# Performance work log

Measured on AMD Instinct MI355X. Metric: run time of the kernel, lower is better.

The kernel has to match this reference:

```python
import jax, jax.numpy as jnp
import numpy as np

N = 50000        # nodes
E = 800000       # edges
IN_C = 128       # in_channels
HID = 256        # hidden_channels
HEADS = 4
HD = HID // HEADS
LAYERS = 4
GRAPHS = 64
OUT_C = 32
MAX_POS = 10
EPS = 1e-5


def layer_norm(x, g, b):
    mu = jnp.mean(x, axis=-1, keepdims=True)
    var = jnp.mean((x - mu) ** 2, axis=-1, keepdims=True)
    return (x - mu) / jnp.sqrt(var + EPS) * g + b


def setup_inputs() -> dict:
    key = jax.random.key(0)
    ks = jax.random.split(key, 32)
    s = 0.02
    inp = {
        "x": jax.random.normal(ks[0], (N, IN_C), dtype=jnp.float32),
        "edge_index": jax.random.randint(ks[1], (2, E), 0, N, dtype=jnp.int32),
        "pos_idx": jax.random.randint(ks[2], (N,), 0, MAX_POS, dtype=jnp.int32),
        "batch": jnp.sort(jax.random.randint(ks[3], (N,), 0, GRAPHS, dtype=jnp.int32)),
        # encoder MLP: Linear(IN->HID), ReLU, LN(HID), Linear(HID->HID); weights stored [in,out]
        "enc_w1": jax.random.normal(ks[4], (IN_C, HID)) * s,
        "enc_b1": jnp.zeros((HID,), jnp.float32),
        "enc_g": jnp.ones((HID,), jnp.float32),
        "enc_beta": jnp.zeros((HID,), jnp.float32),
        "enc_w2": jax.random.normal(ks[5], (HID, HID)) * s,
        "enc_b2": jnp.zeros((HID,), jnp.float32),
        "pos_emb": jax.random.normal(ks[6], (MAX_POS, HID)) * s,
        # stacked attention-layer params [LAYERS, ...]
        "Wq": jax.random.normal(ks[7], (LAYERS, HID, HID)) * s,
        "bq": jnp.zeros((LAYERS, HID), jnp.float32),
        "Wk": jax.random.normal(ks[8], (LAYERS, HID, HID)) * s,
        "bk": jnp.zeros((LAYERS, HID), jnp.float32),
        "Wv": jax.random.normal(ks[9], (LAYERS, HID, HID)) * s,
        "bv": jnp.zeros((LAYERS, HID), jnp.float32),
        "mlp_w1": jax.random.normal(ks[10], (LAYERS, 2 * HID, HID)) * s,
        "mlp_b1": jnp.zeros((LAYERS, HID), jnp.float32),
        "mlp_g": jnp.ones((LAYERS, HID), jnp.float32),
        "mlp_beta": jnp.zeros((LAYERS, HID), jnp.float32),
        "mlp_w2": jax.random.normal(ks[11], (LAYERS, HID, HID)) * s,
        "mlp_b2": jnp.zeros((LAYERS, HID), jnp.float32),
        # classifier
        "cls_w1": jax.random.normal(ks[12], (HID, HID)) * s,
        "cls_b1": jnp.zeros((HID,), jnp.float32),
        "cls_g": jnp.ones((HID,), jnp.float32),
        "cls_beta": jnp.zeros((HID,), jnp.float32),
        "cls_w2": jax.random.normal(ks[13], (HID, OUT_C)) * s,
        "cls_b2": jnp.zeros((OUT_C,), jnp.float32),
    }
    return inp


def reference(x, edge_index, pos_idx, batch,
              enc_w1, enc_b1, enc_g, enc_beta, enc_w2, enc_b2, pos_emb,
              Wq, bq, Wk, bk, Wv, bv,
              mlp_w1, mlp_b1, mlp_g, mlp_beta, mlp_w2, mlp_b2,
              cls_w1, cls_b1, cls_g, cls_beta, cls_w2, cls_b2):
    row, col = edge_index[0], edge_index[1]
    n = x.shape[0]
    e = row.shape[0]

    # NodeEncoder
    h = layer_norm(jax.nn.relu(x @ enc_w1 + enc_b1), enc_g, enc_beta) @ enc_w2 + enc_b2
    h = h + pos_emb[pos_idx]

    scale = jnp.asarray(HD, h.dtype) ** 0.5
    for l in range(LAYERS):
        Q = (h @ Wq[l] + bq[l]).reshape(n, HEADS, HD)
        K = (h @ Wk[l] + bk[l]).reshape(n, HEADS, HD)
        V = (h @ Wv[l] + bv[l]).reshape(n, HEADS, HD)
        # per-edge attention scores [E, HEADS]
        scores = jnp.sum(Q[row] * K[col], axis=-1) / scale
        # segment softmax over destination node `row`
        m = jax.ops.segment_max(scores, row, num_segments=n)
        ex = jnp.exp(scores - m[row])
        denom = jax.ops.segment_sum(ex, row, num_segments=n)
        w = ex / denom[row]                         # [E, HEADS]
        msg = (w[..., None] * V[col]).reshape(e, HID)
        agg = jax.ops.segment_sum(msg, row, num_segments=n)  # [N, HID]
        cat = jnp.concatenate([h, agg], axis=-1)
        z = layer_norm(jax.nn.relu(cat @ mlp_w1[l] + mlp_b1[l]), mlp_g[l], mlp_beta[l]) @ mlp_w2[l] + mlp_b2[l]
        h = z + h

    # global mean pool over graphs
    sums = jax.ops.segment_sum(h, batch, num_segments=GRAPHS)
    cnt = jax.ops.segment_sum(jnp.ones((n, 1), h.dtype), batch, num_segments=GRAPHS)
    pooled = sums / jnp.maximum(cnt, 1.0)

    out = layer_norm(jax.nn.relu(pooled @ cls_w1 + cls_b1), cls_g, cls_beta) @ cls_w2 + cls_b2
    return out
```

## Files before the change

kernel.cpp:

```cpp
#include <hip/hip_runtime.h>
#include <cstdint>

#define HID 256
#define HEADS 4
#define GRAPHS 64
#define OUTC 32
#define EPSV 1e-5f
#define PSPLIT 32

typedef __bf16 b16x8 __attribute__((ext_vector_type(8)));
typedef float  f32x4 __attribute__((ext_vector_type(4)));

__device__ __forceinline__ f32x4 mfma16(b16x8 a, b16x8 b, f32x4 c) {
    return __builtin_amdgcn_mfma_f32_16x16x32_bf16(a, b, c, 0, 0, 0);
}

__device__ __forceinline__ unsigned int pack_bf16(float a, float b) {
    unsigned short ua = __builtin_bit_cast(unsigned short, (__bf16)a);
    unsigned short ub = __builtin_bit_cast(unsigned short, (__bf16)b);
    return (unsigned int)ua | ((unsigned int)ub << 16);
}

__device__ __forceinline__ void unpack2(unsigned int u, float& lo, float& hi) {
    lo = __builtin_bit_cast(float, u << 16);
    hi = __builtin_bit_cast(float, u & 0xffff0000u);
}

__device__ __forceinline__ void stage_gld(char* buf, const unsigned short* __restrict__ src,
                                          int base, int tid)
{
#pragma unroll
    for (int i = 0; i < 8; i++) {
        int idx = i * 256 + tid;
        int r = idx >> 5;
        int u = idx & 31;
        int us = u ^ (r & 7);
        const void* gp = (const void*)(src + (size_t)(base + r) * HID + us * 8);
        __builtin_amdgcn_global_load_lds(
            (const __attribute__((address_space(1))) void*)gp,
            (__attribute__((address_space(3))) void*)(buf + idx * 16),
            16, 0, 0);
    }
}

__global__ __launch_bounds__(256) void wtrans_kernel(const float* __restrict__ W,
    unsigned short* __restrict__ Wt, int K, int C)
{
    __shared__ float tile[32][33];
    const float* Wm = W + (size_t)blockIdx.z * K * C;
    unsigned short* Wtm = Wt + (size_t)blockIdx.z * K * C;
    int k0 = blockIdx.x * 32, c0 = blockIdx.y * 32;
    int tx = threadIdx.x & 31, ty = threadIdx.x >> 5;
#pragma unroll
    for (int i = 0; i < 32; i += 8)
        tile[ty + i][tx] = Wm[(size_t)(k0 + ty + i) * C + c0 + tx];
    __syncthreads();
#pragma unroll
    for (int i = 0; i < 32; i += 8) {
        float v = tile[tx][ty + i];
        Wtm[(size_t)(c0 + ty + i) * K + k0 + tx] =
            __builtin_bit_cast(unsigned short, (__bf16)v);
    }
}

__global__ __launch_bounds__(256) void enc1_mfma(
    const float* __restrict__ in0, const unsigned short* __restrict__ Wt,
    const float* __restrict__ bias, const float* __restrict__ g,
    const float* __restrict__ be, unsigned short* __restrict__ outb, int n)
{
    constexpr int KTILE = 128, ROWB = 256;
    __shared__ __align__(16) char alds[64 * 256];
    __shared__ float red[4][64][2];
    int tid = threadIdx.x, lane = tid & 63, wv = tid >> 6;
    int cg = lane & 15, rg = lane >> 4;
    int base = blockIdx.x * 64;
    int cbase = wv * 64;

    f32x4 acc[4][4];
#pragma unroll
    for (int m = 0; m < 4; m++)
#pragma unroll
        for (int f = 0; f < 4; f++) acc[m][f] = (f32x4){0.f, 0.f, 0.f, 0.f};

#pragma unroll
    for (int i = 0; i < 8; i++) {
        int idx = (i * 256 + tid) * 4;
        int row = idx >> 7, k = idx & 127;
        int node = base + row;
        float4 v = {0.f, 0.f, 0.f, 0.f};
        if (node < n) v = *(const float4*)(in0 + (size_t)node * KTILE + k);
        uint2 pp; pp.x = pack_bf16(v.x, v.y); pp.y = pack_bf16(v.z, v.w);
        int off = row * ROWB + k * 2;
        off ^= (row & 7) << 4;
        *(uint2*)(alds + off) = pp;
    }
    __syncthreads();

#pragma unroll 2
    for (int k0 = 0; k0 < KTILE; k0 += 32) {
        b16x8 a[4], b[4];
#pragma unroll
        for (int m = 0; m < 4; m++) {
            int R = m * 16 + cg;
            int off = R * ROWB + (k0 + rg * 8) * 2;
            off ^= (R & 7) << 4;
            a[m] = __builtin_bit_cast(b16x8, *(const uint4*)(alds + off));
        }
#pragma unroll
        for (int f = 0; f < 4; f++) {
            const unsigned short* p = Wt + (size_t)(cbase + f * 16 + cg) * KTILE + k0 + rg * 8;
            b[f] = __builtin_bit_cast(b16x8, *(const uint4*)p);
        }
#pragma unroll
        for (int m = 0; m < 4; m++)
#pragma unroll
            for (int f = 0; f < 4; f++)
                acc[m][f] = mfma16(a[m], b[f], acc[m][f]);
    }

    float bias_v[4], g_v[4], be_v[4];
#pragma unroll
    for (int f = 0; f < 4; f++) {
        int col = cbase + f * 16 + cg;
        bias_v[f] = bias[col]; g_v[f] = g[col]; be_v[f] = be[col];
    }
#pragma unroll
    for (int m = 0; m < 4; m++)
#pragma unroll
        for (int f = 0; f < 4; f++)
#pragma unroll
            for (int r = 0; r < 4; r++)
                acc[m][f][r] = fmaxf(acc[m][f][r] + bias_v[f], 0.f);
#pragma unroll
    for (int m = 0; m < 4; m++)
#pragma unroll
        for (int r = 0; r < 4; r++) {
            float s = acc[m][0][r] + acc[m][1][r] + acc[m][2][r] + acc[m][3][r];
            float q = acc[m][0][r] * acc[m][0][r] + acc[m][1][r] * acc[m][1][r]
                    + acc[m][2][r] * acc[m][2][r] + acc[m][3][r] * acc[m][3][r];
#pragma unroll
            for (int o = 1; o < 16; o <<= 1) {
                s += __shfl_xor(s, o, 64); q += __shfl_xor(q, o, 64);
            }
            if (cg == 0) { int R = m * 16 + rg * 4 + r; red[wv][R][0] = s; red[wv][R][1] = q; }
        }
    __syncthreads();
#pragma unroll
    for (int m = 0; m < 4; m++)
#pragma unroll
        for (int r = 0; r < 4; r++) {
            int R = m * 16 + rg * 4 + r;
            float S = red[0][R][0] + red[1][R][0] + red[2][R][0] + red[3][R][0];
            float Q = red[0][R][1] + red[1][R][1] + red[2][R][1] + red[3][R][1];
            float mu = S * (1.f / HID);
            float rs = rsqrtf(Q * (1.f / HID) - mu * mu + EPSV);
            int row = base + R;
            if (row >= n) continue;
            size_t ro = (size_t)row * HID;
#pragma unroll
            for (int f = 0; f < 4; f++) {
                float v = (acc[m][f][r] - mu) * rs * g_v[f] + be_v[f];
                outb[ro + cbase + f * 16 + cg] = __builtin_bit_cast(unsigned short, (__bf16)v);
            }
        }
}

template<int NPASS, bool RELU_LN, bool ADD_RES, bool POS, bool OUTF, bool OUTB>
__global__ __launch_bounds__(256) void gemm_bf16(
    const unsigned short* __restrict__ in0, const unsigned short* __restrict__ in1,
    const unsigned short* __restrict__ Wt, const float* __restrict__ bias,
    const float* __restrict__ g, const float* __restrict__ be,
    const float* __restrict__ addsrc, const float* __restrict__ pos_emb,
    const int* __restrict__ pidx, float* __restrict__ outf,
    unsigned short* __restrict__ outb, int n)
{
    constexpr int KTILE = 256;
    constexpr int KS = KTILE * NPASS;
    __shared__ __align__(16) char alds[64 * 512];
    __shared__ float red[4][64][2];

    int tid = threadIdx.x, lane = tid & 63, wv = tid >> 6;
    int cg = lane & 15, rg = lane >> 4;
    int base = blockIdx.x * 64;
    int cbase = wv * 64;

    f32x4 acc[4][4];
#pragma unroll
    for (int m = 0; m < 4; m++)
#pragma unroll
        for (int f = 0; f < 4; f++) acc[m][f] = (f32x4){0.f, 0.f, 0.f, 0.f};

    for (int pass = 0; pass < NPASS; pass++) {
        if (pass) __syncthreads();
        const unsigned short* src = pass ? in1 : in0;
        const unsigned short* Wp = Wt + pass * KTILE;

        stage_gld(alds, src, base, tid);

        b16x8 bcur[4], bnxt[4];
#pragma unroll
        for (int f = 0; f < 4; f++)
            bcur[f] = __builtin_bit_cast(b16x8, *(const uint4*)(
                Wp + (size_t)(cbase + f * 16 + cg) * KS + rg * 8));
        __syncthreads();

#pragma unroll
        for (int kk = 0; kk < 8; kk++) {
            if (kk < 7) {
#pragma unroll
                for (int f = 0; f < 4; f++)
                    bnxt[f] = __builtin_bit_cast(b16x8, *(const uint4*)(
                        Wp + (size_t)(cbase + f * 16 + cg) * KS + (kk + 1) * 32 + rg * 8));
            }
            b16x8 a[4];
#pragma unroll
            for (int m = 0; m < 4; m++) {
                int R = m * 16 + cg;
                int off = R * 512 + (kk * 32 + rg * 8) * 2;
                off ^= (R & 7) << 4;
                a[m] = __builtin_bit_cast(b16x8, *(const uint4*)(alds + off));
            }
#pragma unroll
            for (int m = 0; m < 4; m++)
#pragma unroll
                for (int f = 0; f < 4; f++)
                    acc[m][f] = mfma16(a[m], bcur[f], acc[m][f]);
#pragma unroll
            for (int f = 0; f < 4; f++) bcur[f] = bnxt[f];
        }
    }

    float bias_v[4], g_v[4], be_v[4];
#pragma unroll
    for (int f = 0; f < 4; f++) {
        int col = cbase + f * 16 + cg;
        bias_v[f] = bias[col];
        if (RELU_LN) { g_v[f] = g[col]; be_v[f] = be[col]; }
    }
#pragma unroll
    for (int m = 0; m < 4; m++)
#pragma unroll
        for (int f = 0; f < 4; f++)
#pragma unroll
            for (int r = 0; r < 4; r++) acc[m][f][r] += bias_v[f];

    if (RELU_LN) {
#pragma unroll
        for (int m = 0; m < 4; m++)
#pragma unroll
            for (int f = 0; f < 4; f++)
#pragma unroll
                for (int r = 0; r < 4; r++) acc[m][f][r] = fmaxf(acc[m][f][r], 0.f);
#pragma unroll
        for (int m = 0; m < 4; m++)
#pragma unroll
            for (int r = 0; r < 4; r++) {
                float s = acc[m][0][r] + acc[m][1][r] + acc[m][2][r] + acc[m][3][r];
                float q = acc[m][0][r] * acc[m][0][r] + acc[m][1][r] * acc[m][1][r]
                        + acc[m][2][r] * acc[m][2][r] + acc[m][3][r] * acc[m][3][r];
#pragma unroll
                for (int o = 1; o < 16; o <<= 1) {
                    s += __shfl_xor(s, o, 64); q += __shfl_xor(q, o, 64);
                }
                if (cg == 0) { int R = m * 16 + rg * 4 + r; red[wv][R][0] = s; red[wv][R][1] = q; }
            }
        __syncthreads();
#pragma unroll
        for (int m = 0; m < 4; m++)
#pragma unroll
            for (int r = 0; r < 4; r++) {
                int R = m * 16 + rg * 4 + r;
                float S = red[0][R][0] + red[1][R][0] + red[2][R][0] + red[3][R][0];
                float Q = red[0][R][1] + red[1][R][1] + red[2][R][1] + red[3][R][1];
                float mu = S * (1.f / HID);
                float rs = rsqrtf(Q * (1.f / HID) - mu * mu + EPSV);
#pragma unroll
                for (int f = 0; f < 4; f++)
                    acc[m][f][r] = (acc[m][f][r] - mu) * rs * g_v[f] + be_v[f];
            }
    }

#pragma unroll
    for (int m = 0; m < 4; m++)
#pragma unroll
        for (int r = 0; r < 4; r++) {
            int row = base + m * 16 + rg * 4 + r;
            if (row >= n) continue;
            size_t ro = (size_t)row * HID;
            int pid = 0;
            if (POS) pid = pidx[row];
#pragma unroll
            for (int f = 0; f < 4; f++) {
                int col = cbase + f * 16 + cg;
                float v = acc[m][f][r];
                if (ADD_RES) v += addsrc[ro + col];
                if (POS)     v += pos_emb[(size_t)pid * HID + col];
                if (OUTF)    outf[ro + col] = v;
                if (OUTB)    outb[ro + col] = __builtin_bit_cast(unsigned short, (__bf16)v);
            }
        }
}

__global__ __launch_bounds__(256) void qkv_mfma_kernel(
    const unsigned short* __restrict__ hsrc,
    const unsigned short* __restrict__ Wtq, const unsigned short* __restrict__ Wtk,
    const unsigned short* __restrict__ Wtv,
    const float* __restrict__ bq, const float* __restrict__ bk, const float* __restrict__ bv,
    unsigned short* __restrict__ Qo, unsigned short* __restrict__ Ko,
    unsigned short* __restrict__ Vo, int n)
{
    __shared__ __align__(16) char alds[64 * 512];
    int tid = threadIdx.x, lane = tid & 63, wv = tid >> 6;
    int cg = lane & 15, rg = lane >> 4;
    int base = blockIdx.x * 64;
    int cbase = wv * 64;

    stage_gld(alds, hsrc, base, tid);
    __syncthreads();

    for (int mat = 0; mat < 3; mat++) {
        const unsigned short* Wp = (mat == 0) ? Wtq : (mat == 1) ? Wtk : Wtv;
        const float* bp = (mat == 0) ? bq : (mat == 1) ? bk : bv;
        unsigned short* op = (mat == 0) ? Qo : (mat == 1) ? Ko : Vo;

        f32x4 acc[4][4];
#pragma unroll
        for (int m = 0; m < 4; m++)
#pragma unroll
            for (int f = 0; f < 4; f++) acc[m][f] = (f32x4){0.f, 0.f, 0.f, 0.f};

        b16x8 bcur[4], bnxt[4];
#pragma unroll
        for (int f = 0; f < 4; f++)
            bcur[f] = __builtin_bit_cast(b16x8, *(const uint4*)(
                Wp + (size_t)(cbase + f * 16 + cg) * 256 + rg * 8));

#pragma unroll
        for (int kk = 0; kk < 8; kk++) {
            if (kk < 7) {
#pragma unroll
                for (int f = 0; f < 4; f++)
                    bnxt[f] = __builtin_bit_cast(b16x8, *(const uint4*)(
                        Wp + (size_t)(cbase + f * 16 + cg) * 256 + (kk + 1) * 32 + rg * 8));
            }
            b16x8 a[4];
#pragma unroll
            for (int m = 0; m < 4; m++) {
                int R = m * 16 + cg;
                int off = R * 512 + (kk * 32 + rg * 8) * 2;
                off ^= (R & 7) << 4;
                a[m] = __builtin_bit_cast(b16x8, *(const uint4*)(alds + off));
            }
#pragma unroll
            for (int m = 0; m < 4; m++)
#pragma unroll
                for (int f = 0; f < 4; f++)
                    acc[m][f] = mfma16(a[m], bcur[f], acc[m][f]);
#pragma unroll
            for (int f = 0; f < 4; f++) bcur[f] = bnxt[f];
        }

        float bias_v[4];
#pragma unroll
        for (int f = 0; f < 4; f++) bias_v[f] = bp[cbase + f * 16 + cg];
#pragma unroll
        for (int m = 0; m < 4; m++)
#pragma unroll
            for (int r = 0; r < 4; r++) {
                int row = base + m * 16 + rg * 4 + r;
                if (row >= n) continue;
                size_t ro = (size_t)row * HID;
#pragma unroll
                for (int f = 0; f < 4; f++) {
                    float v = acc[m][f][r] + bias_v[f];
                    op[ro + cbase + f * 16 + cg] = __builtin_bit_cast(unsigned short, (__bf16)v);
                }
            }
    }
}

__global__ void count_kernel(const int* __restrict__ row, int* __restrict__ counts, int e)
{
    int i = blockIdx.x * blockDim.x + threadIdx.x;
    if (i < e) atomicAdd(&counts[row[i]], 1);
}

__global__ __launch_bounds__(256) void scan1_kernel(const int* __restrict__ counts,
    int* __restrict__ offs, int* __restrict__ bsum, int n)
{
    __shared__ int wsumS[4];
    int tid = threadIdx.x, b = blockIdx.x;
    int i = b * 256 + tid;
    int v = (i < n) ? counts[i] : 0;
    int lane = tid & 63, wv = tid >> 6;
    int s = v;
#pragma unroll
    for (int o = 1; o < 64; o <<= 1) { int t = __shfl_up(s, o, 64); if (lane >= o) s += t; }
    if (lane == 63) wsumS[wv] = s;
    __syncthreads();
    int add = 0;
    for (int j = 0; j < wv; j++) add += wsumS[j];
    s += add;
    if (i < n) offs[i + 1] = s;
    if (tid == 255) bsum[b] = s;
}

__global__ __launch_bounds__(256) void scan2_kernel(int* __restrict__ bsum, int nb)
{
    __shared__ int wsumS[4];
    int tid = threadIdx.x;
    int v = (tid < nb) ? bsum[tid] : 0;
    int lane = tid & 63, wv = tid >> 6;
    int s = v;
#pragma unroll
    for (int o = 1; o < 64; o <<= 1) { int t = __shfl_up(s, o, 64); if (lane >= o) s += t; }
    if (lane == 63) wsumS[wv] = s;
    __syncthreads();
    int add = 0;
    for (int j = 0; j < wv; j++) add += wsumS[j];
    s += add;
    if (tid < nb) bsum[tid] = s;
}

__global__ __launch_bounds__(256) void scan3_kernel(int* __restrict__ offs,
    const int* __restrict__ bsum, int n)
{
    int tid = threadIdx.x, b = blockIdx.x;
    int i = b * 256 + tid;
    if (i == 0) offs[0] = 0;
    if (i < n && b > 0) offs[i + 1] += bsum[b - 1];
}

__global__ void scatter_kernel(const int* __restrict__ row, const int* __restrict__ col,
    const int* __restrict__ offs, int* __restrict__ cur, int* __restrict__ ccol, int e)
{
    int i = blockIdx.x * blockDim.x + threadIdx.x;
    if (i >= e) return;
    int r = row[i];
    int pos = atomicAdd(&cur[r], 1);
    ccol[offs[r] + pos] = col[i];
}

__global__ __launch_bounds__(256) void attn_hw_kernel(
    const unsigned short* __restrict__ Qm, const unsigned short* __restrict__ Km,
    const unsigned short* __restrict__ Vm,
    const int* __restrict__ offs, const int* __restrict__ ccol,
    unsigned short* __restrict__ agg, int n)
{
    int tid = threadIdx.x;
    int hw = tid >> 5;
    int l32 = tid & 31;
    int node = blockIdx.x * 8 + hw;
    if (node >= n) return;
    int start = offs[node], fin = offs[node + 1];
    size_t rowoff = (size_t)node * HID + l32 * 8;
    if (start == fin) {
        uint4 z = {0u, 0u, 0u, 0u};
        *(uint4*)(agg + rowoff) = z;
        return;
    }

    uint4 qr = *(const uint4*)(Qm + rowoff);
    float qf[8];
    unpack2(qr.x, qf[0], qf[1]);
    unpack2(qr.y, qf[2], qf[3]);
    unpack2(qr.z, qf[4], qf[5]);
    unpack2(qr.w, qf[6], qf[7]);

    float m = -3.0e38f, d = 0.f;
    float acc[8];
#pragma unroll
    for (int j = 0; j < 8; j++) acc[j] = 0.f;

    for (int i = start; i < fin; i++) {
        int c = ccol[i];
        const unsigned short* kp = Km + (size_t)c * HID + l32 * 8;
        const unsigned short* vp = Vm + (size_t)c * HID + l32 * 8;
        uint4 kr = *(const uint4*)kp;
        uint4 vr = *(const uint4*)vp;
        float k0, k1, k2, k3, k4, k5, k6, k7;
        unpack2(kr.x, k0, k1); unpack2(kr.y, k2, k3);
        unpack2(kr.z, k4, k5); unpack2(kr.w, k6, k7);
        float p = qf[0] * k0 + qf[1] * k1 + qf[2] * k2 + qf[3] * k3
                + qf[4] * k4 + qf[5] * k5 + qf[6] * k6 + qf[7] * k7;
        p += __shfl_xor(p, 1, 64);
        p += __shfl_xor(p, 2, 64);
        p += __shfl_xor(p, 4, 64);
        float s = p * 0.125f;
        float mn = fmaxf(m, s);
        float sc = __expf(m - mn);
        float w = __expf(s - mn);
        d = d * sc + w;
        float v0, v1, v2, v3, v4, v5, v6, v7;
        unpack2(vr.x, v0, v1); unpack2(vr.y, v2, v3);
        unpack2(vr.z, v4, v5); unpack2(vr.w, v6, v7);
        acc[0] = acc[0] * sc + w * v0;  acc[1] = acc[1] * sc + w * v1;
        acc[2] = acc[2] * sc + w * v2;  acc[3] = acc[3] * sc + w * v3;
        acc[4] = acc[4] * sc + w * v4;  acc[5] = acc[5] * sc + w * v5;
        acc[6] = acc[6] * sc + w * v6;  acc[7] = acc[7] * sc + w * v7;
        m = mn;
    }

    float inv = 1.f / d;
    uint4 out;
    out.x = pack_bf16(acc[0] * inv, acc[1] * inv);
    out.y = pack_bf16(acc[2] * inv, acc[3] * inv);
    out.z = pack_bf16(acc[4] * inv, acc[5] * inv);
    out.w = pack_bf16(acc[6] * inv, acc[7] * inv);
    *(uint4*)(agg + rowoff) = out;
}

__global__ void bounds_kernel(const int* __restrict__ batch, int* __restrict__ gb, int n)
{
    int g = threadIdx.x;
    if (g > GRAPHS) return;
    int lo = 0, hi = n;
    while (lo < hi) { int mid = (lo + hi) >> 1; if (batch[mid] < g) lo = mid + 1; else hi = mid; }
    gb[g] = lo;
}

__global__ __launch_bounds__(256) void pool_partial_kernel(const float* __restrict__ h,
    const int* __restrict__ gb, float* __restrict__ partial)
{
    int s = blockIdx.x, g = blockIdx.y, tid = threadIdx.x;
    int lo = gb[g], hi = gb[g + 1];
    float sum = 0.f;
    for (int i = lo + s; i < hi; i += PSPLIT) sum += h[(size_t)i * HID + tid];
    partial[((size_t)g * PSPLIT + s) * HID + tid] = sum;
}

__global__ __launch_bounds__(256) void pool_reduce_kernel(const float* __restrict__ partial,
    const int* __restrict__ gb, float* __restrict__ pooled)
{
    int g = blockIdx.x, tid = threadIdx.x;
    float sum = 0.f;
#pragma unroll
    for (int s = 0; s < PSPLIT; s++) sum += partial[((size_t)g * PSPLIT + s) * HID + tid];
    int cnt = gb[g + 1] - gb[g];
    pooled[g * HID + tid] = sum / fmaxf((float)cnt, 1.f);
}

__global__ __launch_bounds__(256) void cls_kernel(const float* __restrict__ pooled,
    const float* __restrict__ W1, const float* __restrict__ b1,
    const float* __restrict__ g, const float* __restrict__ be,
    const float* __restrict__ W2, const float* __restrict__ b2,
    float* __restrict__ out)
{
    __shared__ float pin[HID];
    __shared__ float hbuf[HID];
    __shared__ float red2[4][2];
    int tid = threadIdx.x, gi = blockIdx.x;
    int lane = tid & 63, wv = tid >> 6;
    pin[tid] = pooled[gi * HID + tid];
    __syncthreads();
    float acc = 0.f;
    for (int k = 0; k < HID; k++) acc += pin[k] * W1[k * HID + tid];
    acc = fmaxf(acc + b1[tid], 0.f);
    float s = acc, q = acc * acc;
#pragma unroll
    for (int o = 1; o < 64; o <<= 1) { s += __shfl_xor(s, o, 64); q += __shfl_xor(q, o, 64); }
    if (lane == 0) { red2[wv][0] = s; red2[wv][1] = q; }
    __syncthreads();
    float S = red2[0][0] + red2[1][0] + red2[2][0] + red2[3][0];
    float Q = red2[0][1] + red2[1][1] + red2[2][1] + red2[3][1];
    float mu = S * (1.f / HID);
    float rs = rsqrtf(Q * (1.f / HID) - mu * mu + EPSV);
    hbuf[tid] = (acc - mu) * rs * g[tid] + be[tid];
    __syncthreads();
    if (tid < OUTC) {
        float o = 0.f;
        for (int k = 0; k < HID; k++) o += hbuf[k] * W2[k * OUTC + tid];
        out[gi * OUTC + tid] = o + b2[tid];
    }
}

extern "C" void kernel_launch(void* const* d_in, const int* in_sizes, int n_in,
                              void* d_out, int out_size, void* d_ws, size_t ws_size,
                              hipStream_t stream)
{
    const float* x        = (const float*)d_in[0];
    const int*   ei       = (const int*)d_in[1];
    const int*   pidx     = (const int*)d_in[2];
    const int*   batch    = (const int*)d_in[3];
    const float* enc_w1   = (const float*)d_in[4];
    const float* enc_b1   = (const float*)d_in[5];
    const float* enc_g    = (const float*)d_in[6];
    const float* enc_beta = (const float*)d_in[7];
    const float* enc_w2   = (const float*)d_in[8];
    const float* enc_b2   = (const float*)d_in[9];
    const float* pos_emb  = (const float*)d_in[10];
    const float* Wq       = (const float*)d_in[11];
    const float* bq       = (const float*)d_in[12];
    const float* Wk       = (const float*)d_in[13];
    const float* bk       = (const float*)d_in[14];
    const float* Wv       = (const float*)d_in[15];
    const float* bv       = (const float*)d_in[16];
    const float* mlp_w1   = (const float*)d_in[17];
    const float* mlp_b1   = (const float*)d_in[18];
    const float* mlp_g    = (const float*)d_in[19];
    const float* mlp_beta = (const float*)d_in[20];
    const float* mlp_w2   = (const float*)d_in[21];
    const float* mlp_b2   = (const float*)d_in[22];
    const float* cls_w1   = (const float*)d_in[23];
    const float* cls_b1   = (const float*)d_in[24];
    const float* cls_g    = (const float*)d_in[25];
    const float* cls_beta = (const float*)d_in[26];
    const float* cls_w2   = (const float*)d_in[27];
    const float* cls_b2   = (const float*)d_in[28];

    int n = in_sizes[2];
    int e = in_sizes[1] / 2;
    const int* row = ei;
    const int* col = ei + e;

    char* p = (char*)d_ws;
    auto alloc = [&](size_t bytes) -> void* {
        void* r = (void*)p;
        p += (bytes + 255) & ~(size_t)255;
        return r;
    };
    size_t NH = (size_t)n * HID;
    float* h             = (float*)alloc(NH * 4);
    unsigned short* h16  = (unsigned short*)alloc(NH * 2);
    unsigned short* a16  = (unsigned short*)alloc(NH * 2);
    unsigned short* m16  = (unsigned short*)alloc(NH * 2);
    unsigned short* Qb   = (unsigned short*)alloc(NH * 2);
    unsigned short* Kb   = (unsigned short*)alloc(NH * 2);
    unsigned short* Vb   = (unsigned short*)alloc(NH * 2);
    float* partial = (float*)alloc((size_t)GRAPHS * PSPLIT * HID * 4);
    float* pooled  = (float*)alloc((size_t)GRAPHS * HID * 4);
    int* counts = (int*)alloc((size_t)n * 4);
    int* offs   = (int*)alloc((size_t)(n + 1) * 4);
    int* cur    = (int*)alloc((size_t)n * 4);
    int* ccol   = (int*)alloc((size_t)e * 4);
    int* bsum   = (int*)alloc(1024);
    int* gb     = (int*)alloc((GRAPHS + 1) * 4);
    unsigned short* wt_e1 = (unsigned short*)alloc((size_t)128 * 256 * 2);
    unsigned short* wt_e2 = (unsigned short*)alloc((size_t)256 * 256 * 2);
    unsigned short* wt_q  = (unsigned short*)alloc((size_t)4 * 256 * 256 * 2);
    unsigned short* wt_k  = (unsigned short*)alloc((size_t)4 * 256 * 256 * 2);
    unsigned short* wt_v  = (unsigned short*)alloc((size_t)4 * 256 * 256 * 2);
    unsigned short* wt_m1 = (unsigned short*)alloc((size_t)4 * 512 * 256 * 2);
    unsigned short* wt_m2 = (unsigned short*)alloc((size_t)4 * 256 * 256 * 2);

    int gblocks = (n + 63) / 64;
    int nb = (n + 255) / 256;

    wtrans_kernel<<<dim3(4, 8, 1),  256, 0, stream>>>(enc_w1, wt_e1, 128, 256);
    wtrans_kernel<<<dim3(8, 8, 1),  256, 0, stream>>>(enc_w2, wt_e2, 256, 256);
    wtrans_kernel<<<dim3(8, 8, 4),  256, 0, stream>>>(Wq,     wt_q,  256, 256);
    wtrans_kernel<<<dim3(8, 8, 4),  256, 0, stream>>>(Wk,     wt_k,  256, 256);
    wtrans_kernel<<<dim3(8, 8, 4),  256, 0, stream>>>(Wv,     wt_v,  256, 256);
    wtrans_kernel<<<dim3(16, 8, 4), 256, 0, stream>>>(mlp_w1, wt_m1, 512, 256);
    wtrans_kernel<<<dim3(8, 8, 4),  256, 0, stream>>>(mlp_w2, wt_m2, 256, 256);

    hipMemsetAsync(counts, 0, (size_t)n * 4, stream);
    hipMemsetAsync(cur, 0, (size_t)n * 4, stream);
    count_kernel<<<(e + 255) / 256, 256, 0, stream>>>(row, counts, e);
    scan1_kernel<<<nb, 256, 0, stream>>>(counts, offs, bsum, n);
    scan2_kernel<<<1, 256, 0, stream>>>(bsum, nb);
    scan3_kernel<<<nb, 256, 0, stream>>>(offs, bsum, n);
    scatter_kernel<<<(e + 255) / 256, 256, 0, stream>>>(row, col, offs, cur, ccol, e);
    bounds_kernel<<<1, 128, 0, stream>>>(batch, gb, n);

    enc1_mfma<<<gblocks, 256, 0, stream>>>(x, wt_e1, enc_b1, enc_g, enc_beta, m16, n);
    gemm_bf16<1, false, false, true, true, true><<<gblocks, 256, 0, stream>>>(
        m16, nullptr, wt_e2, enc_b2, nullptr, nullptr, nullptr, pos_emb, pidx, h, h16, n);

    int ablocks = (n + 7) / 8;
    for (int l = 0; l < 4; l++) {
        size_t wo = (size_t)l * 256 * 256;
        size_t bo = (size_t)l * HID;
        qkv_mfma_kernel<<<gblocks, 256, 0, stream>>>(
            h16, wt_q + wo, wt_k + wo, wt_v + wo, bq + bo, bk + bo, bv + bo,
            Qb, Kb, Vb, n);
        attn_hw_kernel<<<ablocks, 256, 0, stream>>>(Qb, Kb, Vb, offs, ccol, a16, n);
        gemm_bf16<2, true, false, false, false, true><<<gblocks, 256, 0, stream>>>(
            h16, a16, wt_m1 + (size_t)l * 512 * 256, mlp_b1 + bo,
            mlp_g + bo, mlp_beta + bo, nullptr, nullptr, nullptr, nullptr, m16, n);
        gemm_bf16<1, false, true, false, true, true><<<gblocks, 256, 0, stream>>>(
            m16, nullptr, wt_m2 + wo, mlp_b2 + bo, nullptr, nullptr, h, nullptr, nullptr,
            h, h16, n);
    }

    pool_partial_kernel<<<dim3(PSPLIT, GRAPHS), 256, 0, stream>>>(h, gb, partial);
    pool_reduce_kernel<<<GRAPHS, 256, 0, stream>>>(partial, gb, pooled);
    cls_kernel<<<GRAPHS, 256, 0, stream>>>(pooled, cls_w1, cls_b1, cls_g, cls_beta,
                                           cls_w2, cls_b2, (float*)d_out);
}
```

Measured before the change: 1.448 ms.

## Use 128-row GEMM tiles and drop the fp32 residual stream for bf16

The GEMM and QKV kernels now process 128 rows per block as two 64-row sub-tiles that share each B-fragment load. This halves weight-fragment global traffic per row, at the cost of double the accumulator registers, 64KB of LDS per block, and no more B prefetch. The fp32 hidden state is also removed: the residual add reads and writes bf16 h16 in place, and pooling reads bf16. That cuts memory traffic but may lose precision by accumulating the residual in bf16.

```diff
diff --git a/kernel.cpp b/kernel.cpp
--- a/kernel.cpp
+++ b/kernel.cpp
@@ -26,11 +26,15 @@
     hi = __builtin_bit_cast(float, u & 0xffff0000u);
 }
 
-__device__ __forceinline__ void stage_gld(char* buf, const unsigned short* __restrict__ src,
-                                          int base, int tid)
-{
-#pragma unroll
-    for (int i = 0; i < 8; i++) {
+__device__ __forceinline__ float b2f(unsigned short u) {
+    return __builtin_bit_cast(float, (unsigned int)u << 16);
+}
+
+__device__ __forceinline__ void stage_gld128(char* buf, const unsigned short* __restrict__ src,
+                                             int base, int tid)
+{
+#pragma unroll
+    for (int i = 0; i < 16; i++) {
         int idx = i * 256 + tid;
         int r = idx >> 5;
         int u = idx & 31;
@@ -165,68 +169,62 @@
         }
 }
 
-template<int NPASS, bool RELU_LN, bool ADD_RES, bool POS, bool OUTF, bool OUTB>
-__global__ __launch_bounds__(256) void gemm_bf16(
+template<int NPASS, bool RELU_LN, bool ADD_RES, bool POS>
+__global__ __launch_bounds__(256) void gemm128(
     const unsigned short* __restrict__ in0, const unsigned short* __restrict__ in1,
     const unsigned short* __restrict__ Wt, const float* __restrict__ bias,
     const float* __restrict__ g, const float* __restrict__ be,
-    const float* __restrict__ addsrc, const float* __restrict__ pos_emb,
-    const int* __restrict__ pidx, float* __restrict__ outf,
-    unsigned short* __restrict__ outb, int n)
-{
-    constexpr int KTILE = 256;
-    constexpr int KS = KTILE * NPASS;
-    __shared__ __align__(16) char alds[64 * 512];
-    __shared__ float red[4][64][2];
+    const unsigned short* __restrict__ addsrc, const float* __restrict__ pos_emb,
+    const int* __restrict__ pidx, unsigned short* __restrict__ outb, int n)
+{
+    constexpr int KS = 256 * NPASS;
+    __shared__ __align__(16) char alds[128 * 512];
+    __shared__ float red[4][128][2];
 
     int tid = threadIdx.x, lane = tid & 63, wv = tid >> 6;
     int cg = lane & 15, rg = lane >> 4;
-    int base = blockIdx.x * 64;
+    int base = blockIdx.x * 128;
     int cbase = wv * 64;
 
-    f32x4 acc[4][4];
-#pragma unroll
-    for (int m = 0; m < 4; m++)
-#pragma unroll
-        for (int f = 0; f < 4; f++) acc[m][f] = (f32x4){0.f, 0.f, 0.f, 0.f};
+    f32x4 acc[2][4][4];
+#pragma unroll
+    for (int t = 0; t < 2; t++)
+#pragma unroll
+        for (int m = 0; m < 4; m++)
+#pragma unroll
+            for (int f = 0; f < 4; f++) acc[t][m][f] = (f32x4){0.f, 0.f, 0.f, 0.f};
 
     for (int pass = 0; pass < NPASS; pass++) {
         if (pass) __syncthreads();
         const unsigned short* src = pass ? in1 : in0;
-        const unsigned short* Wp = Wt + pass * KTILE;
-
-        stage_gld(alds, src, base, tid);
-
-        b16x8 bcur[4], bnxt[4];
-#pragma unroll
-        for (int f = 0; f < 4; f++)
-            bcur[f] = __builtin_bit_cast(b16x8, *(const uint4*)(
-                Wp + (size_t)(cbase + f * 16 + cg) * KS + rg * 8));
+        const unsigned short* Wp = Wt + pass * 256;
+
+        stage_gld128(alds, src, base, tid);
         __syncthreads();
 
 #pragma unroll
         for (int kk = 0; kk < 8; kk++) {
-            if (kk < 7) {
-#pragma unroll
-                for (int f = 0; f < 4; f++)
-                    bnxt[f] = __builtin_bit_cast(b16x8, *(const uint4*)(
-                        Wp + (size_t)(cbase + f * 16 + cg) * KS + (kk + 1) * 32 + rg * 8));
+            b16x8 b[4];
+#pragma unroll
+            for (int f = 0; f < 4; f++)
+                b[f] = __builtin_bit_cast(b16x8, *(const uint4*)(
+                    Wp + (size_t)(cbase + f * 16 + cg) * KS + kk * 32 + rg * 8));
+#pragma unroll
+            for (int t = 0; t < 2; t++) {
+                b16x8 a[4];
+#pragma unroll
+                for (int m = 0; m < 4; m++) {
+                    int R = t * 64 + m * 16 + cg;
+                    int off = R * 512 + (kk * 32 + rg * 8) * 2;
+                    off ^= (R & 7) << 4;
+                    a[m] = __builtin_bit_cast(b16x8, *(const uint4*)(alds + off));
+                }
+#pragma unroll
+                for (int m = 0; m < 4; m++)
+#pragma unroll
+                    for (int f = 0; f < 4; f++)
+                        acc[t][m][f] = mfma16(a[m], b[f], acc[t][m][f]);
             }
-            b16x8 a[4];
-#pragma unroll
-            for (int m = 0; m < 4; m++) {
-                int R = m * 16 + cg;
-                int off = R * 512 + (kk * 32 + rg * 8) * 2;
-                off ^= (R & 7) << 4;
-                a[m] = __builtin_bit_cast(b16x8, *(const uint4*)(alds + off));
-            }
-#pragma unroll
-            for (int m = 0; m < 4; m++)
-#pragma unroll
-                for (int f = 0; f < 4; f++)
-                    acc[m][f] = mfma16(a[m], bcur[f], acc[m][f]);
-#pragma unroll
-            for (int f = 0; f < 4; f++) bcur[f] = bnxt[f];
         }
     }
 
@@ -238,70 +236,83 @@
         if (RELU_LN) { g_v[f] = g[col]; be_v[f] = be[col]; }
     }
 #pragma unroll
-    for (int m = 0; m < 4; m++)
-#pragma unroll
-        for (int f = 0; f < 4; f++)
-#pragma unroll
-            for (int r = 0; r < 4; r++) acc[m][f][r] += bias_v[f];
+    for (int t = 0; t < 2; t++)
+#pragma unroll
+        for (int m = 0; m < 4; m++)
+#pragma unroll
+            for (int f = 0; f < 4; f++)
+#pragma unroll
+                for (int r = 0; r < 4; r++) acc[t][m][f][r] += bias_v[f];
 
     if (RELU_LN) {
 #pragma unroll
+        for (int t = 0; t < 2; t++)
+#pragma unroll
+            for (int m = 0; m < 4; m++)
+#pragma unroll
+                for (int f = 0; f < 4; f++)
+#pragma unroll
+                    for (int r = 0; r < 4; r++)
+                        acc[t][m][f][r] = fmaxf(acc[t][m][f][r], 0.f);
+#pragma unroll
+        for (int t = 0; t < 2; t++)
+#pragma unroll
+            for (int m = 0; m < 4; m++)
+#pragma unroll
+                for (int r = 0; r < 4; r++) {
+                    float s = acc[t][m][0][r] + acc[t][m][1][r] + acc[t][m][2][r] + acc[t][m][3][r];
+                    float q = acc[t][m][0][r] * acc[t][m][0][r] + acc[t][m][1][r] * acc[t][m][1][r]
+                            + acc[t][m][2][r] * acc[t][m][2][r] + acc[t][m][3][r] * acc[t][m][3][r];
+#pragma unroll
+                    for (int o = 1; o < 16; o <<= 1) {
+                        s += __shfl_xor(s, o, 64); q += __shfl_xor(q, o, 64);
+                    }
+                    if (cg == 0) {
+                        int R = t * 64 + m * 16 + rg * 4 + r;
+                        red[wv][R][0] = s; red[wv][R][1] = q;
+                    }
+                }
+        __syncthreads();
+#pragma unroll
+        for (int t = 0; t < 2; t++)
+#pragma unroll
+            for (int m = 0; m < 4; m++)
+#pragma unroll
+                for (int r = 0; r < 4; r++) {
+                    int R = t * 64 + m * 16 + rg * 4 + r;
+                    float S = red[0][R][0] + red[1][R][0] + red[2][R][0] + red[3][R][0];
+                    float Q = red[0][R][1] + red[1][R][1] + red[2][R][1] + red[3][R][1];
+                    float mu = S * (1.f / HID);
+                    float rs = rsqrtf(Q * (1.f / HID) - mu * mu + EPSV);
+#pragma unroll
+                    for (int f = 0; f < 4; f++)
+                        acc[t][m][f][r] = (acc[t][m][f][r] - mu) * rs * g_v[f] + be_v[f];
+                }
+    }
+
+#pragma unroll
+    for (int t = 0; t < 2; t++)
+#pragma unroll
         for (int m = 0; m < 4; m++)
 #pragma unroll
-            for (int f = 0; f < 4; f++)
-#pragma unroll
-                for (int r = 0; r < 4; r++) acc[m][f][r] = fmaxf(acc[m][f][r], 0.f);
-#pragma unroll
-        for (int m = 0; m < 4; m++)
-#pragma unroll
             for (int r = 0; r < 4; r++) {
-                float s = acc[m][0][r] + acc[m][1][r] + acc[m][2][r] + acc[m][3][r];
-                float q = acc[m][0][r] * acc[m][0][r] + acc[m][1][r] * acc[m][1][r]
-                        + acc[m][2][r] * acc[m][2][r] + acc[m][3][r] * acc[m][3][r];
-#pragma unroll
-                for (int o = 1; o < 16; o <<= 1) {
-                    s += __shfl_xor(s, o, 64); q += __shfl_xor(q, o, 64);
+                int row = base + t * 64 + m * 16 + rg * 4 + r;
+                if (row >= n) continue;
+                size_t ro = (size_t)row * HID;
+                int pid = 0;
+                if (POS) pid = pidx[row];
+#pragma unroll
+                for (int f = 0; f < 4; f++) {
+                    int col = cbase + f * 16 + cg;
+                    float v = acc[t][m][f][r];
+                    if (ADD_RES) v += b2f(addsrc[ro + col]);
+                    if (POS)     v += pos_emb[(size_t)pid * HID + col];
+                    outb[ro + col] = __builtin_bit_cast(unsigned short, (__bf16)v);
                 }
-                if (cg == 0) { int R = m * 16 + rg * 4 + r; red[wv][R][0] = s; red[wv][R][1] = q; }
             }
-        __syncthreads();
-#pragma unroll
-        for (int m = 0; m < 4; m++)
-#pragma unroll
-            for (int r = 0; r < 4; r++) {
-                int R = m * 16 + rg * 4 + r;
-                float S = red[0][R][0] + red[1][R][0] + red[2][R][0] + red[3][R][0];
-                float Q = red[0][R][1] + red[1][R][1] + red[2][R][1] + red[3][R][1];
-                float mu = S * (1.f / HID);
-                float rs = rsqrtf(Q * (1.f / HID) - mu * mu + EPSV);
-#pragma unroll
-                for (int f = 0; f < 4; f++)
-                    acc[m][f][r] = (acc[m][f][r] - mu) * rs * g_v[f] + be_v[f];
-            }
-    }
-
-#pragma unroll
-    for (int m = 0; m < 4; m++)
-#pragma unroll
-        for (int r = 0; r < 4; r++) {
-            int row = base + m * 16 + rg * 4 + r;
-            if (row >= n) continue;
-            size_t ro = (size_t)row * HID;
-            int pid = 0;
-            if (POS) pid = pidx[row];
-#pragma unroll
-            for (int f = 0; f < 4; f++) {
-                int col = cbase + f * 16 + cg;
-                float v = acc[m][f][r];
-                if (ADD_RES) v += addsrc[ro + col];
-                if (POS)     v += pos_emb[(size_t)pid * HID + col];
-                if (OUTF)    outf[ro + col] = v;
-                if (OUTB)    outb[ro + col] = __builtin_bit_cast(unsigned short, (__bf16)v);
-            }
-        }
-}
-
-__global__ __launch_bounds__(256) void qkv_mfma_kernel(
+}
+
+__global__ __launch_bounds__(256) void qkv128_kernel(
     const unsigned short* __restrict__ hsrc,
     const unsigned short* __restrict__ Wtq, const unsigned short* __restrict__ Wtk,
     const unsigned short* __restrict__ Wtv,
@@ -309,13 +320,13 @@
     unsigned short* __restrict__ Qo, unsigned short* __restrict__ Ko,
     unsigned short* __restrict__ Vo, int n)
 {
-    __shared__ __align__(16) char alds[64 * 512];
+    __shared__ __align__(16) char alds[128 * 512];
     int tid = threadIdx.x, lane = tid & 63, wv = tid >> 6;
     int cg = lane & 15, rg = lane >> 4;
-    int base = blockIdx.x * 64;
+    int base = blockIdx.x * 128;
     int cbase = wv * 64;
 
-    stage_gld(alds, hsrc, base, tid);
+    stage_gld128(alds, hsrc, base, tid);
     __syncthreads();
 
     for (int mat = 0; mat < 3; mat++) {
@@ -323,59 +334,58 @@
         const float* bp = (mat == 0) ? bq : (mat == 1) ? bk : bv;
         unsigned short* op = (mat == 0) ? Qo : (mat == 1) ? Ko : Vo;
 
-        f32x4 acc[4][4];
-#pragma unroll
-        for (int m = 0; m < 4; m++)
-#pragma unroll
-            for (int f = 0; f < 4; f++) acc[m][f] = (f32x4){0.f, 0.f, 0.f, 0.f};
-
-        b16x8 bcur[4], bnxt[4];
-#pragma unroll
-        for (int f = 0; f < 4; f++)
-            bcur[f] = __builtin_bit_cast(b16x8, *(const uint4*)(
-                Wp + (size_t)(cbase + f * 16 + cg) * 256 + rg * 8));
+        f32x4 acc[2][4][4];
+#pragma unroll
+        for (int t = 0; t < 2; t++)
+#pragma unroll
+            for (int m = 0; m < 4; m++)
+#pragma unroll
+                for (int f = 0; f < 4; f++) acc[t][m][f] = (f32x4){0.f, 0.f, 0.f, 0.f};
 
 #pragma unroll
         for (int kk = 0; kk < 8; kk++) {
-            if (kk < 7) {
-#pragma unroll
-                for (int f = 0; f < 4; f++)
-                    bnxt[f] = __builtin_bit_cast(b16x8, *(const uint4*)(
-                        Wp + (size_t)(cbase + f * 16 + cg) * 256 + (kk + 1) * 32 + rg * 8));
+            b16x8 b[4];
+#pragma unroll
+            for (int f = 0; f < 4; f++)
+                b[f] = __builtin_bit_cast(b16x8, *(const uint4*)(
+                    Wp + (size_t)(cbase + f * 16 + cg) * 256 + kk * 32 + rg * 8));
+#pragma unroll
+            for (int t = 0; t < 2; t++) {
+                b16x8 a[4];
+#pragma unroll
+                for (int m = 0; m < 4; m++) {
+                    int R = t * 64 + m * 16 + cg;
+                    int off = R * 512 + (kk * 32 + rg * 8) * 2;
+                    off ^= (R & 7) << 4;
+                    a[m] = __builtin_bit_cast(b16x8, *(const uint4*)(alds + off));
+                }
+#pragma unroll
+                for (int m = 0; m < 4; m++)
+#pragma unroll
+                    for (int f = 0; f < 4; f++)
+                        acc[t][m][f] = mfma16(a[m], b[f], acc[t][m][f]);
             }
-            b16x8 a[4];
-#pragma unroll
-            for (int m = 0; m < 4; m++) {
-                int R = m * 16 + cg;
-                int off = R * 512 + (kk * 32 + rg * 8) * 2;
-                off ^= (R & 7) << 4;
-                a[m] = __builtin_bit_cast(b16x8, *(const uint4*)(alds + off));
-            }
+        }
+
+        float bias_v[4];
+#pragma unroll
+        for (int f = 0; f < 4; f++) bias_v[f] = bp[cbase + f * 16 + cg];
+#pragma unroll
+        for (int t = 0; t < 2; t++)
 #pragma unroll
             for (int m = 0; m < 4; m++)
 #pragma unroll
-                for (int f = 0; f < 4; f++)
-                    acc[m][f] = mfma16(a[m], bcur[f], acc[m][f]);
-#pragma unroll
-            for (int f = 0; f < 4; f++) bcur[f] = bnxt[f];
-        }
-
-        float bias_v[4];
-#pragma unroll
-        for (int f = 0; f < 4; f++) bias_v[f] = bp[cbase + f * 16 + cg];
-#pragma unroll
-        for (int m = 0; m < 4; m++)
-#pragma unroll
-            for (int r = 0; r < 4; r++) {
-                int row = base + m * 16 + rg * 4 + r;
-                if (row >= n) continue;
-                size_t ro = (size_t)row * HID;
-#pragma unroll
-                for (int f = 0; f < 4; f++) {
-                    float v = acc[m][f][r] + bias_v[f];
-                    op[ro + cbase + f * 16 + cg] = __builtin_bit_cast(unsigned short, (__bf16)v);
+                for (int r = 0; r < 4; r++) {
+                    int row = base + t * 64 + m * 16 + rg * 4 + r;
+                    if (row >= n) continue;
+                    size_t ro = (size_t)row * HID;
+#pragma unroll
+                    for (int f = 0; f < 4; f++) {
+                        float v = acc[t][m][f][r] + bias_v[f];
+                        op[ro + cbase + f * 16 + cg] =
+                            __builtin_bit_cast(unsigned short, (__bf16)v);
+                    }
                 }
-            }
     }
 }
 
@@ -519,13 +529,15 @@
     gb[g] = lo;
 }
 
-__global__ __launch_bounds__(256) void pool_partial_kernel(const float* __restrict__ h,
+__global__ __launch_bounds__(256) void pool_partial_kernel(
+    const unsigned short* __restrict__ h16,
     const int* __restrict__ gb, float* __restrict__ partial)
 {
     int s = blockIdx.x, g = blockIdx.y, tid = threadIdx.x;
     int lo = gb[g], hi = gb[g + 1];
     float sum = 0.f;
-    for (int i = lo + s; i < hi; i += PSPLIT) sum += h[(size_t)i * HID + tid];
+    for (int i = lo + s; i < hi; i += PSPLIT)
+        sum += b2f(h16[(size_t)i * HID + tid]);
     partial[((size_t)g * PSPLIT + s) * HID + tid] = sum;
 }
 
@@ -620,7 +632,6 @@
         return r;
     };
     size_t NH = (size_t)n * HID;
-    float* h             = (float*)alloc(NH * 4);
     unsigned short* h16  = (unsigned short*)alloc(NH * 2);
     unsigned short* a16  = (unsigned short*)alloc(NH * 2);
     unsigned short* m16  = (unsigned short*)alloc(NH * 2);
@@ -643,7 +654,8 @@
     unsigned short* wt_m1 = (unsigned short*)alloc((size_t)4 * 512 * 256 * 2);
     unsigned short* wt_m2 = (unsigned short*)alloc((size_t)4 * 256 * 256 * 2);
 
-    int gblocks = (n + 63) / 64;
+    int gblocks64  = (n + 63) / 64;
+    int gblocks128 = (n + 127) / 128;
     int nb = (n + 255) / 256;
 
     wtrans_kernel<<<dim3(4, 8, 1),  256, 0, stream>>>(enc_w1, wt_e1, 128, 256);
@@ -663,27 +675,27 @@
     scatter_kernel<<<(e + 255) / 256, 256, 0, stream>>>(row, col, offs, cur, ccol, e);
     bounds_kernel<<<1, 128, 0, stream>>>(batch, gb, n);
 
-    enc1_mfma<<<gblocks, 256, 0, stream>>>(x, wt_e1, enc_b1, enc_g, enc_beta, m16, n);
-    gemm_bf16<1, false, false, true, true, true><<<gblocks, 256, 0, stream>>>(
-        m16, nullptr, wt_e2, enc_b2, nullptr, nullptr, nullptr, pos_emb, pidx, h, h16, n);
+    enc1_mfma<<<gblocks64, 256, 0, stream>>>(x, wt_e1, enc_b1, enc_g, enc_beta, m16, n);
+    gemm128<1, false, false, true><<<gblocks128, 256, 0, stream>>>(
+        m16, nullptr, wt_e2, enc_b2, nullptr, nullptr, nullptr, pos_emb, pidx, h16, n);
 
     int ablocks = (n + 7) / 8;
     for (int l = 0; l < 4; l++) {
         size_t wo = (size_t)l * 256 * 256;
         size_t bo = (size_t)l * HID;
-        qkv_mfma_kernel<<<gblocks, 256, 0, stream>>>(
+        qkv128_kernel<<<gblocks128, 256, 0, stream>>>(
             h16, wt_q + wo, wt_k + wo, wt_v + wo, bq + bo, bk + bo, bv + bo,
             Qb, Kb, Vb, n);
         attn_hw_kernel<<<ablocks, 256, 0, stream>>>(Qb, Kb, Vb, offs, ccol, a16, n);
-        gemm_bf16<2, true, false, false, false, true><<<gblocks, 256, 0, stream>>>(
+        gemm128<2, true, false, false><<<gblocks128, 256, 0, stream>>>(
             h16, a16, wt_m1 + (size_t)l * 512 * 256, mlp_b1 + bo,
-            mlp_g + bo, mlp_beta + bo, nullptr, nullptr, nullptr, nullptr, m16, n);
-        gemm_bf16<1, false, true, false, true, true><<<gblocks, 256, 0, stream>>>(
-            m16, nullptr, wt_m2 + wo, mlp_b2 + bo, nullptr, nullptr, h, nullptr, nullptr,
-            h, h16, n);
-    }
-
-    pool_partial_kernel<<<dim3(PSPLIT, GRAPHS), 256, 0, stream>>>(h, gb, partial);
+            mlp_g + bo, mlp_beta + bo, nullptr, nullptr, nullptr, m16, n);
+        gemm128<1, false, true, false><<<gblocks128, 256, 0, stream>>>(
+            m16, nullptr, wt_m2 + wo, mlp_b2 + bo, nullptr, nullptr, h16, nullptr, nullptr,
+            h16, n);
+    }
+
+    pool_partial_kernel<<<dim3(PSPLIT, GRAPHS), 256, 0, stream>>>(h16, gb, partial);
     pool_reduce_kernel<<<GRAPHS, 256, 0, stream>>>(partial, gb, pooled);
     cls_kernel<<<GRAPHS, 256, 0, stream>>>(pooled, cls_w1, cls_b1, cls_g, cls_beta,
                                            cls_w2, cls_b2, (float*)d_out);
```

New measurement: 1.241 ms. 14.3% less time.
